# Kernel optimization log

Hardware: AMD Instinct MI355X
Metric: run time of the kernel (lower is better)

The kernel has to match this reference:

```python
import jax, jax.numpy as jnp
import numpy as np

NUM_TERMS = 3
HIDDEN = 64
CLAMP_MIN = 1e-10


def _hermite_basis(x, num_terms):
    hs = [jnp.ones_like(x)]
    if num_terms > 1:
        hs.append(2.0 * x)
    for n in range(1, num_terms - 1):
        hs.append(2.0 * x * hs[n] - 2.0 * n * hs[n - 1])
    return jnp.stack(hs[:num_terms], axis=-1)  # (..., num_terms)


def setup_inputs() -> dict:
    key = jax.random.key(0)
    ks = jax.random.split(key, 7)
    B, S = 2048, 1024
    ys_coeffs = jax.random.normal(ks[0], (B, S, 2), dtype=jnp.float32)
    # scoring MLP params: Linear(3,64) -> ReLU -> Linear(64,64) -> ReLU -> Linear(64,num_terms)
    def lin(k, fan_in, fan_out):
        bound = 1.0 / np.sqrt(fan_in)
        kw, kb = jax.random.split(k)
        W = jax.random.uniform(kw, (fan_in, fan_out), minval=-bound, maxval=bound, dtype=jnp.float32)
        b = jax.random.uniform(kb, (fan_out,), minval=-bound, maxval=bound, dtype=jnp.float32)
        return W, b
    W1, b1 = lin(ks[1], 3, HIDDEN)
    W2, b2 = lin(ks[2], HIDDEN, HIDDEN)
    Wout, bout = lin(ks[3], HIDDEN, NUM_TERMS)
    return {"ys_coeffs": ys_coeffs, "W1": W1, "b1": b1, "W2": W2, "b2": b2,
            "Wout": Wout, "bout": bout}


def reference(ys_coeffs, W1, b1, W2, b2, Wout, bout):
    B, S, _ = ys_coeffs.shape
    timestamps = ys_coeffs[:, :, 0]
    values = ys_coeffs[:, :, 1]
    x0 = values[:, :-1]            # (B, S-1)
    xt = values[:, 1:]             # (B, S-1)
    t = timestamps[:, 1:]          # (B, S-1)
    feats = jnp.stack([xt, t, x0], axis=-1)           # (B, S-1, 3)
    h1 = jax.nn.relu(feats @ W1 + b1)                 # (B, S-1, 64)
    h2 = jax.nn.relu(h1 @ W2 + b2)                    # (B, S-1, 64)
    c_n = h2 @ Wout + bout                            # (B, S-1, num_terms)
    herm = _hermite_basis(xt, NUM_TERMS)              # (B, S-1, num_terms)
    p = jnp.sum(c_n * herm, axis=-1)                  # (B, S-1)
    p = jax.nn.softmax(p, axis=0)                     # softmax over batch dim (as in torch dim=0)
    log_likelihood = jnp.log(jnp.clip(p, CLAMP_MIN)).sum(axis=-1)  # (B,)
    return log_likelihood.mean()
```

## Files before the change

### kernel.cpp

```cpp
#include <hip/hip_runtime.h>
#include <hip/hip_bf16.h>

#define HIDDEN 64
#define BATCH 2048
#define SFULL 1024
#define SM1 1023
#define LN_CLAMP -23.025850929940457f
#define PAIRS 8

typedef __bf16 bf16x8 __attribute__((ext_vector_type(8)));
typedef float  f32x4  __attribute__((ext_vector_type(4)));

#define FRAG_UNITS 19
#define FRAG_BYTES (FRAG_UNITS * 64 * 16)

__device__ __forceinline__ int permrow(int rho) {
    return 32 * ((rho >> 4) >> 1) + 8 * ((rho >> 2) & 3) + 4 * ((rho >> 4) & 1) + (rho & 3);
}

__global__ __launch_bounds__(256) void frag_setup_kernel(
    const float* __restrict__ W1, const float* __restrict__ b1,
    const float* __restrict__ W2, const float* __restrict__ b2,
    const float* __restrict__ Wout, const float* __restrict__ bout,
    char* __restrict__ F)
{
    const int lane = threadIdx.x & 63;
    const int wv   = threadIdx.x >> 6;
    const int col  = lane & 15;
    const int g    = lane >> 4;

    if (wv == 0) {
#pragma unroll
        for (int mt = 0; mt < 4; ++mt) {
            const int p2 = permrow(16 * mt + col);
            bf16x8 v;
#pragma unroll
            for (int j = 0; j < 8; ++j) {
                const int k = 8 * g + j;
                v[j] = (k < 3) ? (__bf16)W1[k * 64 + p2]
                     : (k == 3) ? (__bf16)b1[p2] : (__bf16)0.0f;
            }
            *(bf16x8*)(F + ((mt * 64 + lane) << 4)) = v;
        }
#pragma unroll
        for (int c = 0; c < 2; ++c) {
            bf16x8 v;
#pragma unroll
            for (int j = 0; j < 8; ++j)
                v[j] = (col < 3) ? (__bf16)Wout[(32 * c + 8 * g + j) * 3 + col] : (__bf16)0.0f;
            *(bf16x8*)(F + (((12 + c) * 64 + lane) << 4)) = v;
        }
        f32x4 c3 = {0.f, 0.f, 0.f, 0.f};
        if (g == 0) { c3[0] = bout[0]; c3[1] = bout[1]; c3[2] = bout[2]; }
        *(f32x4*)(F + ((18 * 64 + lane) << 4)) = c3;
    } else if (wv == 1 || wv == 2) {
#pragma unroll
        for (int m = 0; m < 2; ++m) {
            const int mt = (wv - 1) * 2 + m;
            const int p2 = permrow(16 * mt + col);
#pragma unroll
            for (int c = 0; c < 2; ++c) {
                bf16x8 v;
#pragma unroll
                for (int j = 0; j < 8; ++j)
                    v[j] = (__bf16)W2[(32 * c + 8 * g + j) * 64 + p2];
                *(bf16x8*)(F + (((4 + mt * 2 + c) * 64 + lane) << 4)) = v;
            }
        }
    } else {
#pragma unroll
        for (int mt = 0; mt < 4; ++mt) {
            f32x4 v;
#pragma unroll
            for (int r = 0; r < 4; ++r)
                v[r] = b2[permrow(16 * mt + 4 * g + r)];
            *(f32x4*)(F + (((14 + mt) * 64 + lane) << 4)) = v;
        }
    }
}

__global__ __launch_bounds__(256, 3) void mlp_z_kernel(
    const float* __restrict__ ys,
    const char* __restrict__ F,
    float* __restrict__ z)
{
    const int lane = threadIdx.x & 63;
    const int wv   = threadIdx.x >> 6;
    const int col  = lane & 15;

    const int b   = (blockIdx.x * 4 + wv) * 16 + col;
    const int sp0 = blockIdx.y * (2 * PAIRS);
    const int omax = (SFULL - 1) - sp0;

    bf16x8 a1[4], a2[4][2], a3[2];
    f32x4 c2init[4], c3init;
#pragma unroll
    for (int mt = 0; mt < 4; ++mt) {
        a1[mt]       = *(const bf16x8*)(F + ((mt * 64 + lane) << 4));
        a2[mt][0]    = *(const bf16x8*)(F + (((4 + mt * 2) * 64 + lane) << 4));
        a2[mt][1]    = *(const bf16x8*)(F + (((5 + mt * 2) * 64 + lane) << 4));
        c2init[mt]   = *(const f32x4*)(F + (((14 + mt) * 64 + lane) << 4));
    }
    a3[0]  = *(const bf16x8*)(F + ((12 * 64 + lane) << 4));
    a3[1]  = *(const bf16x8*)(F + ((13 * 64 + lane) << 4));
    c3init = *(const f32x4*)(F + ((18 * 64 + lane) << 4));

    const f32x4 zero4 = {0.f, 0.f, 0.f, 0.f};

    const float2* base2 = reinterpret_cast<const float2*>(ys) + ((size_t)b * SFULL + sp0);
    float* zb = z + (size_t)sp0 * BATCH + b;

    float2 qa = base2[0];
    float2 qb = base2[1];
    float2 qc = base2[2];

    for (int it = 0; it < PAIRS; ++it) {
        const int o1n = min(2 * it + 3, omax);
        const int o2n = min(2 * it + 4, omax);
        const float2 nb = base2[o1n];
        const float2 nc = base2[o2n];

        const float x0a = qa.y, ta = qb.x, xta = qb.y;
        const float x0b = qb.y, tb = qc.x, xtb = qc.y;

        bf16x8 f0a, f0b;
        f0a[0] = (__bf16)xta; f0a[1] = (__bf16)ta;
        f0a[2] = (__bf16)x0a; f0a[3] = (__bf16)1.0f;
        f0a[4] = f0a[0]; f0a[5] = f0a[1]; f0a[6] = f0a[2]; f0a[7] = f0a[3];
        f0b[0] = (__bf16)xtb; f0b[1] = (__bf16)tb;
        f0b[2] = (__bf16)x0b; f0b[3] = (__bf16)1.0f;
        f0b[4] = f0b[0]; f0b[5] = f0b[1]; f0b[6] = f0b[2]; f0b[7] = f0b[3];

        f32x4 acc1a[4], acc1b[4];
#pragma unroll
        for (int mt = 0; mt < 4; ++mt) {
            acc1a[mt] = __builtin_amdgcn_mfma_f32_16x16x32_bf16(a1[mt], f0a, zero4, 0, 0, 0);
            acc1b[mt] = __builtin_amdgcn_mfma_f32_16x16x32_bf16(a1[mt], f0b, zero4, 0, 0, 0);
        }

        bf16x8 hfa[2], hfb[2];
#pragma unroll
        for (int c = 0; c < 2; ++c)
#pragma unroll
            for (int j = 0; j < 8; ++j) {
                hfa[c][j] = (__bf16)fmaxf(acc1a[2 * c + (j >> 2)][j & 3], 0.0f);
                hfb[c][j] = (__bf16)fmaxf(acc1b[2 * c + (j >> 2)][j & 3], 0.0f);
            }

        f32x4 acc2a[4], acc2b[4];
#pragma unroll
        for (int mt = 0; mt < 4; ++mt) {
            acc2a[mt] = __builtin_amdgcn_mfma_f32_16x16x32_bf16(a2[mt][0], hfa[0], c2init[mt], 0, 0, 0);
            acc2b[mt] = __builtin_amdgcn_mfma_f32_16x16x32_bf16(a2[mt][0], hfb[0], c2init[mt], 0, 0, 0);
        }
#pragma unroll
        for (int mt = 0; mt < 4; ++mt) {
            acc2a[mt] = __builtin_amdgcn_mfma_f32_16x16x32_bf16(a2[mt][1], hfa[1], acc2a[mt], 0, 0, 0);
            acc2b[mt] = __builtin_amdgcn_mfma_f32_16x16x32_bf16(a2[mt][1], hfb[1], acc2b[mt], 0, 0, 0);
        }

        bf16x8 h2fa[2], h2fb[2];
#pragma unroll
        for (int c = 0; c < 2; ++c)
#pragma unroll
            for (int j = 0; j < 8; ++j) {
                h2fa[c][j] = (__bf16)fmaxf(acc2a[2 * c + (j >> 2)][j & 3], 0.0f);
                h2fb[c][j] = (__bf16)fmaxf(acc2b[2 * c + (j >> 2)][j & 3], 0.0f);
            }

        f32x4 acc3a, acc3b;
        acc3a = __builtin_amdgcn_mfma_f32_16x16x32_bf16(a3[0], h2fa[0], c3init, 0, 0, 0);
        acc3b = __builtin_amdgcn_mfma_f32_16x16x32_bf16(a3[0], h2fb[0], c3init, 0, 0, 0);
        acc3a = __builtin_amdgcn_mfma_f32_16x16x32_bf16(a3[1], h2fa[1], acc3a, 0, 0, 0);
        acc3b = __builtin_amdgcn_mfma_f32_16x16x32_bf16(a3[1], h2fb[1], acc3b, 0, 0, 0);

        const float zva = fmaf(acc3a[2], fmaf(4.0f * xta, xta, -2.0f),
                          fmaf(acc3a[1], xta + xta, acc3a[0]));
        const float zvb = fmaf(acc3b[2], fmaf(4.0f * xtb, xtb, -2.0f),
                          fmaf(acc3b[1], xtb + xtb, acc3b[0]));

        if (lane < 16) {
            zb[(size_t)(2 * it) * BATCH] = zva;
            if (sp0 + 2 * it + 1 < SM1)
                zb[(size_t)(2 * it + 1) * BATCH] = zvb;
        }

        qa = qc; qb = nb; qc = nc;
    }
}

__device__ __forceinline__ float blk_reduce_max(float v) {
    __shared__ float s[4];
#pragma unroll
    for (int off = 32; off >= 1; off >>= 1) v = fmaxf(v, __shfl_xor(v, off));
    if ((threadIdx.x & 63) == 0) s[threadIdx.x >> 6] = v;
    __syncthreads();
    v = fmaxf(fmaxf(s[0], s[1]), fmaxf(s[2], s[3]));
    __syncthreads();
    return v;
}

__device__ __forceinline__ float blk_reduce_sum(float v) {
    __shared__ float s[4];
#pragma unroll
    for (int off = 32; off >= 1; off >>= 1) v += __shfl_xor(v, off);
    if ((threadIdx.x & 63) == 0) s[threadIdx.x >> 6] = v;
    __syncthreads();
    v = (s[0] + s[1]) + (s[2] + s[3]);
    __syncthreads();
    return v;
}

__global__ __launch_bounds__(256) void col_softmax_kernel(
    const float* __restrict__ z, float* __restrict__ colsum)
{
    const int sp = blockIdx.x;
    const int tid = threadIdx.x;
    const float* col = z + (size_t)sp * BATCH;

    float vals[8];
    float m = -3.4e38f;
#pragma unroll
    for (int i = 0; i < 8; ++i) {
        vals[i] = col[tid + 256 * i];
        m = fmaxf(m, vals[i]);
    }
    const float M = blk_reduce_max(m);

    float se = 0.0f;
#pragma unroll
    for (int i = 0; i < 8; ++i) se += __expf(vals[i] - M);
    const float S = blk_reduce_sum(se);
    const float L = __logf(S);

    float acc = 0.0f;
#pragma unroll
    for (int i = 0; i < 8; ++i) acc += fmaxf(vals[i] - M - L, LN_CLAMP);
    const float T = blk_reduce_sum(acc);
    if (tid == 0) colsum[sp] = T;
}

__global__ __launch_bounds__(256) void final_reduce_kernel(
    const float* __restrict__ colsum, float* __restrict__ out)
{
    const int tid = threadIdx.x;
    float v = 0.0f;
    for (int i = tid; i < SM1; i += 256) v += colsum[i];
    const float T = blk_reduce_sum(v);
    if (tid == 0) out[0] = T / (float)BATCH;
}

extern "C" void kernel_launch(void* const* d_in, const int* in_sizes, int n_in,
                              void* d_out, int out_size, void* d_ws, size_t ws_size,
                              hipStream_t stream) {
    const float* ys   = (const float*)d_in[0];
    const float* W1   = (const float*)d_in[1];
    const float* b1   = (const float*)d_in[2];
    const float* W2   = (const float*)d_in[3];
    const float* b2   = (const float*)d_in[4];
    const float* Wout = (const float*)d_in[5];
    const float* bout = (const float*)d_in[6];
    float* out = (float*)d_out;

    float* z      = (float*)d_ws;
    float* colsum = z + (size_t)SM1 * BATCH;
    size_t fo = ((size_t)SM1 * BATCH + SM1) * sizeof(float);
    fo = (fo + 15) & ~(size_t)15;
    char* F = (char*)d_ws + fo;

    frag_setup_kernel<<<1, 256, 0, stream>>>(W1, b1, W2, b2, Wout, bout, F);
    dim3 grid1(32, 64);
    mlp_z_kernel<<<grid1, 256, 0, stream>>>(ys, F, z);
    col_softmax_kernel<<<SM1, 256, 0, stream>>>(z, colsum);
    final_reduce_kernel<<<1, 256, 0, stream>>>(colsum, out);
}
```

Before: 49.91 us.

## Stage MLP weight fragments in LDS and process one position per iteration

Weight fragments move from per-thread registers into shared memory and are re-read from LDS on every iteration, cutting register pressure so launch bounds can request 4 blocks per SM instead of 3. The loop now handles a single sequence position per iteration rather than interleaving two. The float-to-bf16 conversion plus ReLU uses a byte-perm truncation and a packed 16-bit integer max. This trades the instruction-level parallelism of the two interleaved chains for more resident waves, and it adds LDS traffic on every iteration. The truncating conversion also changes rounding slightly compared with the original casts.

```diff
diff --git a/kernel.cpp b/kernel.cpp
--- a/kernel.cpp
+++ b/kernel.cpp
@@ -6,16 +6,43 @@
 #define SFULL 1024
 #define SM1 1023
 #define LN_CLAMP -23.025850929940457f
-#define PAIRS 8
+#define SP_PER 16
 
 typedef __bf16 bf16x8 __attribute__((ext_vector_type(8)));
 typedef float  f32x4  __attribute__((ext_vector_type(4)));
 
 #define FRAG_UNITS 19
-#define FRAG_BYTES (FRAG_UNITS * 64 * 16)
 
 __device__ __forceinline__ int permrow(int rho) {
     return 32 * ((rho >> 4) >> 1) + 8 * ((rho >> 2) & 3) + 4 * ((rho >> 4) & 1) + (rho & 3);
+}
+
+__device__ __forceinline__ unsigned pkt(float lo, float hi) {
+    return __builtin_amdgcn_perm(__float_as_uint(hi), __float_as_uint(lo), 0x07060302u);
+}
+typedef short s16x2 __attribute__((ext_vector_type(2)));
+__device__ __forceinline__ unsigned rp(unsigned x) {
+    s16x2 v = __builtin_bit_cast(s16x2, x);
+    s16x2 z = {0, 0};
+    v = __builtin_elementwise_max(v, z);
+    return __builtin_bit_cast(unsigned, v);
+}
+
+__device__ __forceinline__ bf16x8 relu_pack2(const f32x4 a, const f32x4 b) {
+    union { unsigned u[4]; bf16x8 v; } r;
+    r.u[0] = rp(pkt(a[0], a[1]));
+    r.u[1] = rp(pkt(a[2], a[3]));
+    r.u[2] = rp(pkt(b[0], b[1]));
+    r.u[3] = rp(pkt(b[2], b[3]));
+    return r.v;
+}
+
+__device__ __forceinline__ bf16x8 featpk(float xt, float t, float x0) {
+    union { unsigned u[4]; bf16x8 v; } r;
+    r.u[0] = pkt(xt, t);
+    r.u[1] = pkt(x0, 1.0f);
+    r.u[2] = r.u[0]; r.u[3] = r.u[1];
+    return r.v;
 }
 
 __global__ __launch_bounds__(256) void frag_setup_kernel(
@@ -79,113 +106,94 @@
     }
 }
 
-__global__ __launch_bounds__(256, 3) void mlp_z_kernel(
+__global__ __launch_bounds__(256, 4) void mlp_z_kernel(
     const float* __restrict__ ys,
     const char* __restrict__ F,
     float* __restrict__ z)
 {
-    const int lane = threadIdx.x & 63;
+    __shared__ __align__(16) char Flds[14 * 64 * 16];
+
+    const int l    = threadIdx.x & 63;
     const int wv   = threadIdx.x >> 6;
-    const int col  = lane & 15;
+    const int col  = l & 15;
+
+    for (int i = threadIdx.x; i < 14 * 64; i += 256)
+        *(f32x4*)(Flds + ((size_t)i << 4)) = *(const f32x4*)(F + ((size_t)i << 4));
 
     const int b   = (blockIdx.x * 4 + wv) * 16 + col;
-    const int sp0 = blockIdx.y * (2 * PAIRS);
+    const int sp0 = blockIdx.y * SP_PER;
     const int omax = (SFULL - 1) - sp0;
 
-    bf16x8 a1[4], a2[4][2], a3[2];
     f32x4 c2init[4], c3init;
 #pragma unroll
-    for (int mt = 0; mt < 4; ++mt) {
-        a1[mt]       = *(const bf16x8*)(F + ((mt * 64 + lane) << 4));
-        a2[mt][0]    = *(const bf16x8*)(F + (((4 + mt * 2) * 64 + lane) << 4));
-        a2[mt][1]    = *(const bf16x8*)(F + (((5 + mt * 2) * 64 + lane) << 4));
-        c2init[mt]   = *(const f32x4*)(F + (((14 + mt) * 64 + lane) << 4));
-    }
-    a3[0]  = *(const bf16x8*)(F + ((12 * 64 + lane) << 4));
-    a3[1]  = *(const bf16x8*)(F + ((13 * 64 + lane) << 4));
-    c3init = *(const f32x4*)(F + ((18 * 64 + lane) << 4));
+    for (int mt = 0; mt < 4; ++mt)
+        c2init[mt] = *(const f32x4*)(F + (((14 + mt) * 64 + l) << 4));
+    c3init = *(const f32x4*)(F + ((18 * 64 + l) << 4));
 
     const f32x4 zero4 = {0.f, 0.f, 0.f, 0.f};
 
     const float2* base2 = reinterpret_cast<const float2*>(ys) + ((size_t)b * SFULL + sp0);
     float* zb = z + (size_t)sp0 * BATCH + b;
 
-    float2 qa = base2[0];
-    float2 qb = base2[1];
-    float2 qc = base2[2];
-
-    for (int it = 0; it < PAIRS; ++it) {
-        const int o1n = min(2 * it + 3, omax);
-        const int o2n = min(2 * it + 4, omax);
-        const float2 nb = base2[o1n];
-        const float2 nc = base2[o2n];
-
-        const float x0a = qa.y, ta = qb.x, xta = qb.y;
-        const float x0b = qb.y, tb = qc.x, xtb = qc.y;
-
-        bf16x8 f0a, f0b;
-        f0a[0] = (__bf16)xta; f0a[1] = (__bf16)ta;
-        f0a[2] = (__bf16)x0a; f0a[3] = (__bf16)1.0f;
-        f0a[4] = f0a[0]; f0a[5] = f0a[1]; f0a[6] = f0a[2]; f0a[7] = f0a[3];
-        f0b[0] = (__bf16)xtb; f0b[1] = (__bf16)tb;
-        f0b[2] = (__bf16)x0b; f0b[3] = (__bf16)1.0f;
-        f0b[4] = f0b[0]; f0b[5] = f0b[1]; f0b[6] = f0b[2]; f0b[7] = f0b[3];
-
-        f32x4 acc1a[4], acc1b[4];
-#pragma unroll
-        for (int mt = 0; mt < 4; ++mt) {
-            acc1a[mt] = __builtin_amdgcn_mfma_f32_16x16x32_bf16(a1[mt], f0a, zero4, 0, 0, 0);
-            acc1b[mt] = __builtin_amdgcn_mfma_f32_16x16x32_bf16(a1[mt], f0b, zero4, 0, 0, 0);
-        }
-
-        bf16x8 hfa[2], hfb[2];
-#pragma unroll
-        for (int c = 0; c < 2; ++c)
-#pragma unroll
-            for (int j = 0; j < 8; ++j) {
-                hfa[c][j] = (__bf16)fmaxf(acc1a[2 * c + (j >> 2)][j & 3], 0.0f);
-                hfb[c][j] = (__bf16)fmaxf(acc1b[2 * c + (j >> 2)][j & 3], 0.0f);
-            }
-
-        f32x4 acc2a[4], acc2b[4];
-#pragma unroll
-        for (int mt = 0; mt < 4; ++mt) {
-            acc2a[mt] = __builtin_amdgcn_mfma_f32_16x16x32_bf16(a2[mt][0], hfa[0], c2init[mt], 0, 0, 0);
-            acc2b[mt] = __builtin_amdgcn_mfma_f32_16x16x32_bf16(a2[mt][0], hfb[0], c2init[mt], 0, 0, 0);
-        }
-#pragma unroll
-        for (int mt = 0; mt < 4; ++mt) {
-            acc2a[mt] = __builtin_amdgcn_mfma_f32_16x16x32_bf16(a2[mt][1], hfa[1], acc2a[mt], 0, 0, 0);
-            acc2b[mt] = __builtin_amdgcn_mfma_f32_16x16x32_bf16(a2[mt][1], hfb[1], acc2b[mt], 0, 0, 0);
-        }
-
-        bf16x8 h2fa[2], h2fb[2];
-#pragma unroll
-        for (int c = 0; c < 2; ++c)
-#pragma unroll
-            for (int j = 0; j < 8; ++j) {
-                h2fa[c][j] = (__bf16)fmaxf(acc2a[2 * c + (j >> 2)][j & 3], 0.0f);
-                h2fb[c][j] = (__bf16)fmaxf(acc2b[2 * c + (j >> 2)][j & 3], 0.0f);
-            }
-
-        f32x4 acc3a, acc3b;
-        acc3a = __builtin_amdgcn_mfma_f32_16x16x32_bf16(a3[0], h2fa[0], c3init, 0, 0, 0);
-        acc3b = __builtin_amdgcn_mfma_f32_16x16x32_bf16(a3[0], h2fb[0], c3init, 0, 0, 0);
-        acc3a = __builtin_amdgcn_mfma_f32_16x16x32_bf16(a3[1], h2fa[1], acc3a, 0, 0, 0);
-        acc3b = __builtin_amdgcn_mfma_f32_16x16x32_bf16(a3[1], h2fb[1], acc3b, 0, 0, 0);
-
-        const float zva = fmaf(acc3a[2], fmaf(4.0f * xta, xta, -2.0f),
-                          fmaf(acc3a[1], xta + xta, acc3a[0]));
-        const float zvb = fmaf(acc3b[2], fmaf(4.0f * xtb, xtb, -2.0f),
-                          fmaf(acc3b[1], xtb + xtb, acc3b[0]));
-
-        if (lane < 16) {
-            zb[(size_t)(2 * it) * BATCH] = zva;
-            if (sp0 + 2 * it + 1 < SM1)
-                zb[(size_t)(2 * it + 1) * BATCH] = zvb;
-        }
-
-        qa = qc; qb = nb; qc = nc;
+    float2 q0 = base2[0];
+    float2 q1 = base2[min(1, omax)];
+    float2 qn = base2[min(2, omax)];
+
+    __syncthreads();
+
+    for (int it = 0; it < SP_PER; ++it) {
+        unsigned loff = (unsigned)(l << 4);
+        asm volatile("" : "+v"(loff));
+#define LDSF(u) (*(const bf16x8*)(Flds + ((u) * 1024) + loff))
+
+        const float2 qn2 = base2[min(it + 3, omax)];
+
+        const float x0 = q0.y, t = q1.x, xt = q1.y;
+        const bf16x8 f0 = featpk(xt, t, x0);
+
+        bf16x8 w10 = LDSF(0), w11 = LDSF(1), w12 = LDSF(2), w13 = LDSF(3);
+        f32x4 acc1[4];
+        acc1[0] = __builtin_amdgcn_mfma_f32_16x16x32_bf16(w10, f0, zero4, 0, 0, 0);
+        acc1[1] = __builtin_amdgcn_mfma_f32_16x16x32_bf16(w11, f0, zero4, 0, 0, 0);
+        acc1[2] = __builtin_amdgcn_mfma_f32_16x16x32_bf16(w12, f0, zero4, 0, 0, 0);
+        acc1[3] = __builtin_amdgcn_mfma_f32_16x16x32_bf16(w13, f0, zero4, 0, 0, 0);
+
+        bf16x8 w200 = LDSF(4), w210 = LDSF(6), w220 = LDSF(8), w230 = LDSF(10);
+
+        bf16x8 hf[2];
+        hf[0] = relu_pack2(acc1[0], acc1[1]);
+        hf[1] = relu_pack2(acc1[2], acc1[3]);
+
+        f32x4 acc2[4];
+        acc2[0] = __builtin_amdgcn_mfma_f32_16x16x32_bf16(w200, hf[0], c2init[0], 0, 0, 0);
+        acc2[1] = __builtin_amdgcn_mfma_f32_16x16x32_bf16(w210, hf[0], c2init[1], 0, 0, 0);
+        acc2[2] = __builtin_amdgcn_mfma_f32_16x16x32_bf16(w220, hf[0], c2init[2], 0, 0, 0);
+        acc2[3] = __builtin_amdgcn_mfma_f32_16x16x32_bf16(w230, hf[0], c2init[3], 0, 0, 0);
+
+        bf16x8 w201 = LDSF(5), w211 = LDSF(7), w221 = LDSF(9), w231 = LDSF(11);
+        acc2[0] = __builtin_amdgcn_mfma_f32_16x16x32_bf16(w201, hf[1], acc2[0], 0, 0, 0);
+        acc2[1] = __builtin_amdgcn_mfma_f32_16x16x32_bf16(w211, hf[1], acc2[1], 0, 0, 0);
+        acc2[2] = __builtin_amdgcn_mfma_f32_16x16x32_bf16(w221, hf[1], acc2[2], 0, 0, 0);
+        acc2[3] = __builtin_amdgcn_mfma_f32_16x16x32_bf16(w231, hf[1], acc2[3], 0, 0, 0);
+
+        bf16x8 w30 = LDSF(12), w31 = LDSF(13);
+
+        bf16x8 h2f[2];
+        h2f[0] = relu_pack2(acc2[0], acc2[1]);
+        h2f[1] = relu_pack2(acc2[2], acc2[3]);
+
+        f32x4 acc3;
+        acc3 = __builtin_amdgcn_mfma_f32_16x16x32_bf16(w30, h2f[0], c3init, 0, 0, 0);
+        acc3 = __builtin_amdgcn_mfma_f32_16x16x32_bf16(w31, h2f[1], acc3, 0, 0, 0);
+#undef LDSF
+
+        const float zv = fmaf(acc3[2], fmaf(4.0f * xt, xt, -2.0f),
+                         fmaf(acc3[1], xt + xt, acc3[0]));
+
+        if (l < 16 && sp0 + it < SM1)
+            zb[(size_t)it * BATCH] = zv;
+
+        q0 = q1; q1 = qn; qn = qn2;
     }
 }
 
```

Measured after the change: 45.45 us. 8.9% less time.
